# Kernel optimization log

Measured on AMD Instinct MI355X. Metric: run time of the kernel, lower is better.

## Reference

```python
import jax, jax.numpy as jnp
import numpy as np

# dims (match init_kwargs)
T, B, N, D_OB = 256, 32, 64, 4
D_MODEL = N * D_OB            # 256
D_PE = 16
D_T = D_MODEL + D_PE          # 272 transformer width
H = 8
DH = D_T // H                 # 34
L = 2
DFF = 1024
C = 2
MAX_LEN = T
F_IN = T * D_OB               # 1024, ObservationPropagation channels


def setup_inputs() -> dict:
    key = jax.random.key(0)
    ks = jax.random.split(key, 24)
    g = lambda k, shp: 0.02 * jax.random.normal(k, shp, dtype=jnp.float32)
    return {
        "x": jax.random.normal(ks[0], (T, B, N), dtype=jnp.float32),
        "times": jnp.sort(jax.random.uniform(ks[1], (T, B), dtype=jnp.float32) * MAX_LEN, axis=0),
        "lengths": jax.random.randint(ks[2], (B,), MAX_LEN // 2, MAX_LEN + 1),
        "R_u": g(ks[3], (1, N * D_OB)),
        "Wv1": g(ks[4], (F_IN, F_IN)), "bv1": g(ks[5], (F_IN,)),
        "Wv2": g(ks[6], (F_IN, F_IN)), "bv2": g(ks[7], (F_IN,)),
        "qkv_w": g(ks[8], (L, D_T, 3 * D_T)), "qkv_b": g(ks[9], (L, 3 * D_T)),
        "out_w": g(ks[10], (L, D_T, D_T)), "out_b": g(ks[11], (L, D_T)),
        "ln1_w": jnp.ones((L, D_T), jnp.float32), "ln1_b": jnp.zeros((L, D_T), jnp.float32),
        "ln2_w": jnp.ones((L, D_T), jnp.float32), "ln2_b": jnp.zeros((L, D_T), jnp.float32),
        "ffn_w1": g(ks[12], (L, D_T, DFF)), "ffn_b1": g(ks[13], (L, DFF)),
        "ffn_w2": g(ks[14], (L, DFF, D_T)), "ffn_b2": g(ks[15], (L, D_T)),
        "mlp_w1": g(ks[16], (D_T, D_T)), "mlp_b1": g(ks[17], (D_T,)),
        "mlp_w2": g(ks[18], (D_T, C)), "mlp_b2": g(ks[19], (C,)),
    }


def _pos_encode(times):
    # PositionalEncodingTF: timescales = max_len ** linspace(0,1,d_pe//2)
    scales = MAX_LEN ** np.linspace(0.0, 1.0, D_PE // 2)
    st = times[..., None] / jnp.asarray(scales, times.dtype)  # [T,B,8]
    return jnp.concatenate([jnp.sin(st), jnp.cos(st)], axis=-1)  # [T,B,16]


def _segment_softmax(w, seg, num_segments):
    m = jax.ops.segment_max(w, seg, num_segments=num_segments)
    e = jnp.exp(w - m[seg])
    s = jax.ops.segment_sum(e, seg, num_segments=num_segments)
    return e / s[seg]


def _ob_propagate(xn, src, tgt, edge_w, Wv, bv):
    """Batched ObservationPropagation (use_beta=False, decompose=False).
    xn: [B,N,F]; messages = relu(lin_value(x_src)) * softmax(edge_w per target);
    scatter-add at targets. Returns (out, pre-softmax alpha == edge_w)."""
    gamma = _segment_softmax(edge_w, tgt, N)              # [E]
    value = jax.nn.relu(xn @ Wv + bv)                     # [B,N,F] (linear commutes with gather)
    msg = value[:, src, :] * gamma[None, :, None]         # [B,E,F] -- dominant memory traffic
    out = jnp.zeros_like(xn).at[:, tgt, :].add(msg)       # segment-sum at target nodes
    return out, edge_w


def _ln(x, w, b):
    mu = jnp.mean(x, axis=-1, keepdims=True)
    var = jnp.mean((x - mu) ** 2, axis=-1, keepdims=True)
    return (x - mu) / jnp.sqrt(var + 1e-5) * w + b


def _encoder_layer(xt, key_pad, qkv_w, qkv_b, out_w, out_b, ln1_w, ln1_b, ln2_w, ln2_b, w1, b1, w2, b2):
    # xt: [T,B,D_T]; key_pad: [B,T] True = padded. Post-norm torch TransformerEncoderLayer, relu, no dropout.
    Tt, Bb, _ = xt.shape
    q, k, v = jnp.split(xt @ qkv_w + qkv_b, 3, axis=-1)
    to_h = lambda t: t.reshape(Tt, Bb, H, DH).transpose(1, 2, 0, 3)  # [B,H,T,dh]
    scores = jnp.einsum("bhqd,bhkd->bhqk", to_h(q), to_h(k)) / jnp.sqrt(jnp.asarray(DH, xt.dtype))
    scores = jnp.where(key_pad[:, None, None, :], -jnp.inf, scores)
    attn = jax.nn.softmax(scores, axis=-1)
    o = jnp.einsum("bhqk,bhkd->bhqd", attn, to_h(v)).transpose(2, 0, 1, 3).reshape(Tt, Bb, D_T)
    xt = _ln(xt + o @ out_w + out_b, ln1_w, ln1_b)
    ff = jax.nn.relu(xt @ w1 + b1) @ w2 + b2
    return _ln(xt + ff, ln2_w, ln2_b)


def _forward(x, times, lengths, R_u, Wv1, bv1, Wv2, bv2, qkv_w, qkv_b, out_w, out_b,
             ln1_w, ln1_b, ln2_w, ln2_b, ffn_w1, ffn_b1, ffn_w2, ffn_b2,
             mlp_w1, mlp_b1, mlp_w2, mlp_b2):
    Bb = x.shape[1]
    # observation embedding: repeat each sensor d_ob times, scale by R_u, relu
    h = jax.nn.relu(jnp.repeat(x, D_OB, axis=-1) * R_u)          # [T,B,N*d_ob]
    pe = _pos_encode(times)                                      # [T,B,16]
    key_pad = jnp.arange(T)[None, :] >= lengths[:, None]         # [B,T]
    # reshape to per-sensor node features: [B, N, T*d_ob]
    xn = h.reshape(T, Bb, N, D_OB).transpose(1, 2, 0, 3).reshape(Bb, N, F_IN)
    # dense all-pairs graph (global_structure = ones); torch.nonzero order is row-major
    src = jnp.repeat(jnp.arange(N), N)   # edge_index[0]
    tgt = jnp.tile(jnp.arange(N), N)     # edge_index[1] (aggregation index)
    ew = jnp.ones((N * N,), x.dtype)
    xn, ew2 = _ob_propagate(xn, src, tgt, ew, Wv1, bv1)
    xn, _ = _ob_propagate(xn, src, tgt, ew2, Wv2, bv2)
    out = xn.reshape(Bb, N, T, D_OB).transpose(2, 0, 1, 3).reshape(T, Bb, N * D_OB)
    out = jnp.concatenate([out, pe], axis=2)                     # [T,B,272]
    for l in range(L):
        out = _encoder_layer(out, key_pad, qkv_w[l], qkv_b[l], out_w[l], out_b[l],
                             ln1_w[l], ln1_b[l], ln2_w[l], ln2_b[l],
                             ffn_w1[l], ffn_b1[l], ffn_w2[l], ffn_b2[l])
    keep = (~key_pad).T[:, :, None].astype(out.dtype)            # [T,B,1]
    agg = jnp.sum(out * keep, axis=0) / (lengths[:, None].astype(out.dtype) + 1.0)
    hid = jax.nn.relu(agg @ mlp_w1 + mlp_b1)
    logits = hid @ mlp_w2 + mlp_b2
    return jax.nn.softmax(logits, axis=1)                        # [B,C]


def reference(x, times, lengths, R_u, Wv1, bv1, Wv2, bv2, qkv_w, qkv_b, out_w, out_b,
              ln1_w, ln1_b, ln2_w, ln2_b, ffn_w1, ffn_b1, ffn_w2, ffn_b2,
              mlp_w1, mlp_b1, mlp_w2, mlp_b2):
    return _forward(x, times, lengths, R_u, Wv1, bv1, Wv2, bv2, qkv_w, qkv_b, out_w, out_b,
                    ln1_w, ln1_b, ln2_w, ln2_b, ffn_w1, ffn_b1, ffn_w2, ffn_b2,
                    mlp_w1, mlp_b1, mlp_w2, mlp_b2)
```

## Files before the change

### kernel.cpp

```cpp
#include <hip/hip_runtime.h>
#include <math.h>

#define T_DIM 256
#define B_DIM 32
#define N_DIM 64
#define F_INF 1024
#define D_T 272
#define D_TP 288
#define H_DIM 8
#define DH_DIM 34
#define DFF_DIM 1024

typedef unsigned int uint;
typedef short bf16x8 __attribute__((ext_vector_type(8)));
typedef float f32x4 __attribute__((ext_vector_type(4)));

__device__ __forceinline__ ushort f2bf(float f) {
    uint u = __float_as_uint(f);
    uint r = (u + 0x7fffu + ((u >> 16) & 1u)) >> 16;
    return (ushort)r;
}
__device__ __forceinline__ float bf2f(ushort u) {
    return __uint_as_float(((uint)u) << 16);
}

struct WT {
    int tstart[11];
    const float* src[10];
    ushort* dst[10];
    int K[10];
    int N[10];
    int Kp[10];
    int ntn[10];
};
__global__ __launch_bounds__(256) void wconv_tiled(WT s) {
    int tile = blockIdx.x;
    int seg = 0;
    while (seg < 9 && tile >= s.tstart[seg + 1]) ++seg;
    int ti = tile - s.tstart[seg];
    int ntn = s.ntn[seg];
    int tk = ti / ntn, tn = ti - tk * ntn;
    int N = s.N[seg], Kp = s.Kp[seg];
    __shared__ float t[16][17];
    int ty = threadIdx.x >> 4, tx = threadIdx.x & 15;
    t[ty][tx] = s.src[seg][(size_t)(tk * 16 + ty) * N + tn * 16 + tx];
    __syncthreads();
    s.dst[seg][(size_t)(tn * 16 + ty) * Kp + tk * 16 + tx] = f2bf(t[tx][ty]);
}

struct PadPtrs {
    uint* wt[6];
    int nrows[6];
};
__global__ void init_kernel(const float* __restrict__ x, const float* __restrict__ Ru,
                            ushort* __restrict__ xn, uint* __restrict__ qkvb,
                            uint* __restrict__ x1, uint* __restrict__ attno, PadPtrs p) {
    const int TB = T_DIM * B_DIM;
    const int NXN = B_DIM * N_DIM * F_INF;
    int idx = blockIdx.x * blockDim.x + threadIdx.x;
    if (idx < NXN) {
        int f = idx & 1023;
        int bn = idx >> 10;
        int n = bn & 63;
        int b = bn >> 6;
        int t = f >> 2;
        int d = f & 3;
        float v = x[(t * B_DIM + b) * N_DIM + n] * Ru[(n << 2) + d];
        xn[idx] = f2bf(fmaxf(v, 0.0f));
        return;
    }
    idx -= NXN;
    if (idx < TB * 8) {
        int row = idx >> 3, q = idx & 7;
        x1[(size_t)row * 144 + 136 + q] = 0;
        attno[(size_t)row * 144 + 136 + q] = 0;
        return;
    }
    idx -= TB * 8;
    if (idx < TB * 72) {
        int row = idx / 72;
        int r = idx - row * 72;
        int g = r / 3, q = r - g * 3;
        qkvb[(size_t)row * 480 + g * 20 + 17 + q] = 0;
        return;
    }
    idx -= TB * 72;
#pragma unroll
    for (int sgi = 0; sgi < 6; ++sgi) {
        int cnt = p.nrows[sgi] * 8;
        if (idx < cnt) {
            int row = idx >> 3, q = idx & 7;
            p.wt[sgi][(size_t)row * 144 + 136 + q] = 0;
            return;
        }
        idx -= cnt;
    }
}

template <int ACT, int OUT_MODE>
__global__ __launch_bounds__(256) void gemm_mfma(const ushort* __restrict__ A,
                                                 const ushort* __restrict__ Bt,
                                                 const float* __restrict__ bias,
                                                 void* __restrict__ Cout,
                                                 int M, int N, int K, int Kstride) {
    __shared__ ushort As[3][64 * 32];
    __shared__ ushort Bs[3][128 * 32];
    const int tid = threadIdx.x;
    const int m0 = (OUT_MODE == 3) ? 0 : blockIdx.y * 64;
    const int n0 = blockIdx.x * 128;
    if (OUT_MODE == 3) {
        A += (size_t)blockIdx.y * K;
        Bt += (size_t)blockIdx.y * K;
    }
    const int w = tid >> 6, lane = tid & 63;
    const int wr = w >> 1, wc = w & 1;
    const int lr = lane & 15, lk = lane >> 4;

    const int ns = K >> 5;

    const int ra = w * 16 + (lane >> 2);
    const int ca = (((lane & 3) ^ ((ra >> 1) & 3)) << 3);
    int gma = m0 + ra; if (gma > M - 1) gma = M - 1;
    const ushort* gA = &A[(size_t)gma * Kstride + ca];
    const int rb0 = w * 32 + (lane >> 2);
    const int cb0 = (((lane & 3) ^ ((rb0 >> 1) & 3)) << 3);
    const int rb1 = rb0 + 16;
    const int cb1 = (((lane & 3) ^ ((rb1 >> 1) & 3)) << 3);
    int gnb0 = n0 + rb0; if (gnb0 > N - 1) gnb0 = N - 1;
    int gnb1 = n0 + rb1; if (gnb1 > N - 1) gnb1 = N - 1;
    const ushort* gB0 = &Bt[(size_t)gnb0 * Kstride + cb0];
    const ushort* gB1 = &Bt[(size_t)gnb1 * Kstride + cb1];

    f32x4 acc[2][4];
#pragma unroll
    for (int i = 0; i < 2; ++i)
#pragma unroll
        for (int j = 0; j < 4; ++j) acc[i][j] = (f32x4){0.f, 0.f, 0.f, 0.f};

    auto stage = [&](int buf, int s) {
        const int k0 = s << 5;
        __builtin_amdgcn_global_load_lds(
            (const __attribute__((address_space(1))) void*)(gA + k0),
            (__attribute__((address_space(3))) void*)(&As[buf][w * 512]), 16, 0, 0);
        __builtin_amdgcn_global_load_lds(
            (const __attribute__((address_space(1))) void*)(gB0 + k0),
            (__attribute__((address_space(3))) void*)(&Bs[buf][w * 1024]), 16, 0, 0);
        __builtin_amdgcn_global_load_lds(
            (const __attribute__((address_space(1))) void*)(gB1 + k0),
            (__attribute__((address_space(3))) void*)(&Bs[buf][w * 1024 + 512]), 16, 0, 0);
    };

    stage(0, 0);
    stage(1, 1);
    asm volatile("s_waitcnt vmcnt(3)" ::: "memory");
    __builtin_amdgcn_sched_barrier(0);
    __builtin_amdgcn_s_barrier();
    __builtin_amdgcn_sched_barrier(0);

    int cur = 0;
    for (int s = 0; s < ns; ++s) {
        int stg = cur + 2; if (stg >= 3) stg -= 3;
        if (s + 2 < ns) stage(stg, s + 2);

        bf16x8 af[2], bf[4];
#pragma unroll
        for (int mt = 0; mt < 2; ++mt) {
            int row = wr * 32 + mt * 16 + lr;
            int ch = lk ^ ((row >> 1) & 3);
            af[mt] = *reinterpret_cast<const bf16x8*>(&As[cur][row * 32 + ch * 8]);
        }
#pragma unroll
        for (int nt = 0; nt < 4; ++nt) {
            int row = wc * 64 + nt * 16 + lr;
            int ch = lk ^ ((row >> 1) & 3);
            bf[nt] = *reinterpret_cast<const bf16x8*>(&Bs[cur][row * 32 + ch * 8]);
        }
        __builtin_amdgcn_s_setprio(1);
#pragma unroll
        for (int mt = 0; mt < 2; ++mt)
#pragma unroll
            for (int nt = 0; nt < 4; ++nt)
                acc[mt][nt] = __builtin_amdgcn_mfma_f32_16x16x32_bf16(
                    af[mt], bf[nt], acc[mt][nt], 0, 0, 0);
        __builtin_amdgcn_s_setprio(0);

        if (s + 1 < ns) {
            if (s + 2 < ns)
                asm volatile("s_waitcnt vmcnt(3)" ::: "memory");
            else
                asm volatile("s_waitcnt vmcnt(0)" ::: "memory");
            __builtin_amdgcn_sched_barrier(0);
            __builtin_amdgcn_s_barrier();
            __builtin_amdgcn_sched_barrier(0);
        }
        cur = (cur == 2) ? 0 : cur + 1;
    }

    if (OUT_MODE == 4) {
        __shared__ float red[2][128];
        float part[4];
#pragma unroll
        for (int nt = 0; nt < 4; ++nt) {
            int col = n0 + wc * 64 + nt * 16 + lr;
            float bv = bias[col];
            float s = 0.f;
#pragma unroll
            for (int mt = 0; mt < 2; ++mt)
#pragma unroll
                for (int r = 0; r < 4; ++r) s += fmaxf(acc[mt][nt][r] + bv, 0.f);
            s += __shfl_xor(s, 16);
            s += __shfl_xor(s, 32);
            part[nt] = s;
        }
        if (lk == 0) {
#pragma unroll
            for (int nt = 0; nt < 4; ++nt) red[wr][wc * 64 + nt * 16 + lr] = part[nt];
        }
        __syncthreads();
        if (tid < 128) {
            float tot = red[0][tid] + red[1][tid];
            ((ushort*)Cout)[(size_t)blockIdx.y * 1024 + n0 + tid] =
                f2bf(tot * (1.0f / 64.0f));
        }
        return;
    }

#pragma unroll
    for (int nt = 0; nt < 4; ++nt) {
        int col = n0 + wc * 64 + nt * 16 + lr;
        if (col >= N) continue;
        float bv = (OUT_MODE == 3) ? 0.f : bias[col];
        int g = 0, dcol = 0;
        if (OUT_MODE == 2) { g = col / 34; dcol = col - g * 34; }
#pragma unroll
        for (int mt = 0; mt < 2; ++mt) {
#pragma unroll
            for (int r = 0; r < 4; ++r) {
                int row = m0 + wr * 32 + mt * 16 + lk * 4 + r;
                if (row >= M) continue;
                float v = acc[mt][nt][r] + bv;
                if (ACT == 1) v = fmaxf(v, 0.0f);
                if (OUT_MODE == 0)
                    ((float*)Cout)[(size_t)row * N + col] = v;
                else if (OUT_MODE == 1)
                    ((ushort*)Cout)[(size_t)row * N + col] = f2bf(v);
                else if (OUT_MODE == 2)
                    ((ushort*)Cout)[(size_t)row * 960 + g * 40 + dcol] = f2bf(v);
                else
                    ((float*)Cout)[(size_t)(blockIdx.y * M + row) * N + col] = v;
            }
        }
    }
}

__global__ __launch_bounds__(256) void gemm_ln(const ushort* __restrict__ A,
                                               const ushort* __restrict__ Bt,
                                               const float* __restrict__ bias,
                                               const ushort* __restrict__ resid,
                                               const float* __restrict__ lnw,
                                               const float* __restrict__ lnb,
                                               ushort* __restrict__ Out,
                                               int K, int Kstride) {
    __shared__ ushort lds[32256];
    const int tid = threadIdx.x;
    const int m0 = blockIdx.x * 64;
    const int w = tid >> 6, lane = tid & 63;
    const int lr = lane & 15, lk = lane >> 4;
    const int ns = K >> 5;

    const int ra = w * 16 + (lane >> 2);
    const int ca = (((lane & 3) ^ ((ra >> 1) & 3)) << 3);
    const ushort* gA = &A[(size_t)(m0 + ra) * Kstride + ca];

    f32x4 acc[17];
#pragma unroll
    for (int t = 0; t < 17; ++t) acc[t] = (f32x4){0.f, 0.f, 0.f, 0.f};

    auto stage = [&](int buf, int s) {
        const int k0 = s << 5;
        __builtin_amdgcn_global_load_lds(
            (const __attribute__((address_space(1))) void*)(gA + k0),
            (__attribute__((address_space(3))) void*)(&lds[buf * 2048 + w * 512]),
            16, 0, 0);
        for (int c = w; c < 17; c += 4) {
            int row16 = c * 16 + (lane >> 2);
            int p8 = (((lane & 3) ^ ((row16 >> 1) & 3)) << 3);
            const ushort* src = &Bt[(size_t)row16 * Kstride + k0 + p8];
            __builtin_amdgcn_global_load_lds(
                (const __attribute__((address_space(1))) void*)src,
                (__attribute__((address_space(3))) void*)(&lds[6144 + buf * 8704 + c * 512]),
                16, 0, 0);
        }
    };

    stage(0, 0);
    stage(1, 1);
    if (w == 0)
        asm volatile("s_waitcnt vmcnt(6)" ::: "memory");
    else
        asm volatile("s_waitcnt vmcnt(5)" ::: "memory");
    __builtin_amdgcn_sched_barrier(0);
    __builtin_amdgcn_s_barrier();
    __builtin_amdgcn_sched_barrier(0);

    int cur = 0;
    for (int s = 0; s < ns; ++s) {
        int stg = cur + 2; if (stg >= 3) stg -= 3;
        if (s + 2 < ns) stage(stg, s + 2);

        bf16x8 af;
        {
            int row = w * 16 + lr;
            int ch = lk ^ ((row >> 1) & 3);
            af = *reinterpret_cast<const bf16x8*>(&lds[cur * 2048 + row * 32 + ch * 8]);
        }
        __builtin_amdgcn_s_setprio(1);
#pragma unroll
        for (int t = 0; t < 17; ++t) {
            int row = t * 16 + lr;
            int ch = lk ^ ((row >> 1) & 3);
            bf16x8 bf = *reinterpret_cast<const bf16x8*>(
                &lds[6144 + cur * 8704 + row * 32 + ch * 8]);
            acc[t] = __builtin_amdgcn_mfma_f32_16x16x32_bf16(af, bf, acc[t], 0, 0, 0);
        }
        __builtin_amdgcn_s_setprio(0);

        if (s + 1 < ns) {
            if (s + 2 < ns) {
                if (w == 0)
                    asm volatile("s_waitcnt vmcnt(6)" ::: "memory");
                else
                    asm volatile("s_waitcnt vmcnt(5)" ::: "memory");
            } else {
                asm volatile("s_waitcnt vmcnt(0)" ::: "memory");
            }
            __builtin_amdgcn_sched_barrier(0);
            __builtin_amdgcn_s_barrier();
            __builtin_amdgcn_sched_barrier(0);
        }
        cur = (cur == 2) ? 0 : cur + 1;
    }

    __syncthreads();
    for (int i = tid; i < 64 * 34; i += 256) {
        int row = i / 34, c8 = i - row * 34;
        *reinterpret_cast<uint4*>(&lds[row * 272 + c8 * 8]) =
            *reinterpret_cast<const uint4*>(&resid[(size_t)(m0 + row) * D_TP + c8 * 8]);
    }
    __syncthreads();

    float sum[4] = {0.f, 0.f, 0.f, 0.f}, sq[4] = {0.f, 0.f, 0.f, 0.f};
#pragma unroll
    for (int t = 0; t < 17; ++t) {
        int col = t * 16 + lr;
        float bv = bias[col];
#pragma unroll
        for (int r = 0; r < 4; ++r) {
            int row = w * 16 + lk * 4 + r;
            float v = acc[t][r] + bv + bf2f(lds[row * 272 + col]);
            acc[t][r] = v;
            sum[r] += v;
            sq[r] += v * v;
        }
    }
#pragma unroll
    for (int mask = 1; mask <= 8; mask <<= 1)
#pragma unroll
        for (int r = 0; r < 4; ++r) {
            sum[r] += __shfl_xor(sum[r], mask);
            sq[r] += __shfl_xor(sq[r], mask);
        }
    float mu[4], inv[4];
#pragma unroll
    for (int r = 0; r < 4; ++r) {
        mu[r] = sum[r] * (1.0f / D_T);
        float var = sq[r] * (1.0f / D_T) - mu[r] * mu[r];
        inv[r] = 1.0f / sqrtf(var + 1e-5f);
    }
#pragma unroll
    for (int t = 0; t < 17; ++t) {
        int col = t * 16 + lr;
        float wv = lnw[col], bb = lnb[col];
#pragma unroll
        for (int r = 0; r < 4; ++r) {
            int row = m0 + w * 16 + lk * 4 + r;
            Out[(size_t)row * D_TP + col] = f2bf((acc[t][r] - mu[r]) * inv[r] * wv + bb);
        }
    }
}

__global__ __launch_bounds__(256) void reduce_p2_kernel(const float* __restrict__ part,
                                                        const float* __restrict__ bv2,
                                                        float* __restrict__ out2) {
    int idx = blockIdx.x * 256 + threadIdx.x;
    if (idx >= B_DIM * F_INF) return;
    int g = idx & 1023;
    float s = bv2[g];
#pragma unroll
    for (int ks = 0; ks < 4; ++ks) s += part[(size_t)ks * B_DIM * F_INF + idx];
    out2[idx] = fmaxf(s, 0.f);
}

__global__ void seq_kernel(const float* __restrict__ out2, const float* __restrict__ times,
                           ushort* __restrict__ seq) {
    int idx = blockIdx.x * blockDim.x + threadIdx.x;
    if (idx >= T_DIM * B_DIM * D_TP) return;
    int c = idx % D_TP;
    int tb = idx / D_TP;
    float v;
    if (c < 256) {
        v = out2[(tb % B_DIM) * 1024 + ((tb / B_DIM) << 2) + (c & 3)];
    } else if (c < 272) {
        int s = c - 256;
        int sc = (s < 8) ? s : s - 8;
        float arg = times[tb] * exp2f(-8.0f * (float)sc * (1.0f / 7.0f));
        v = (s < 8) ? sinf(arg) : cosf(arg);
    } else {
        v = 0.f;
    }
    seq[idx] = f2bf(v);
}

__global__ __launch_bounds__(256) void attn_mfma(const ushort* __restrict__ qkv,
                                                 const int* __restrict__ lengths,
                                                 ushort* __restrict__ attno) {
    const int b = blockIdx.x >> 3;
    const int h = blockIdx.x & 7;
    const int tid = threadIdx.x;
    const int w = tid >> 6, lane = tid & 63;
    const int lr = lane & 15, lk = lane >> 4;
    __shared__ ushort Ks[2][64 * 40];
    __shared__ ushort Vt[2][48 * 72];
    __shared__ ushort Ps[4][64 * 72];
    const int len = lengths[b];
    const float scale = 0.1714985851f;
    const bf16x8 zv = {0, 0, 0, 0, 0, 0, 0, 0};

    for (int i = tid; i < 2 * 8 * 72; i += 256) {
        int bb = i / 576;
        Vt[bb][40 * 72 + (i - bb * 576)] = 0;
    }

    const int srow0 = tid / 5, sch0 = tid - srow0 * 5;
    const int srow1 = (tid + 256) / 5, sch1 = (tid + 256) - srow1 * 5;
    const int sjp0 = (srow0 & 15) * 4 + (srow0 >> 4);
    const int sjp1 = (srow1 & 15) * 4 + (srow1 >> 4);
    const bool has1 = (tid < 64);
    bf16x8 kreg0, kreg1, vreg0, vreg1;

    auto LOADS = [&](int c) {
        const ushort* b0 = &qkv[(size_t)((c * 64 + srow0) * 32 + b) * 960 + h * 40];
        kreg0 = *reinterpret_cast<const bf16x8*>(b0 + 320 + sch0 * 8);
        vreg0 = *reinterpret_cast<const bf16x8*>(b0 + 640 + sch0 * 8);
        if (has1) {
            const ushort* b1 = &qkv[(size_t)((c * 64 + srow1) * 32 + b) * 960 + h * 40];
            kreg1 = *reinterpret_cast<const bf16x8*>(b1 + 320 + sch1 * 8);
            vreg1 = *reinterpret_cast<const bf16x8*>(b1 + 640 + sch1 * 8);
        }
    };
    auto WRITES = [&](int buf) {
        *reinterpret_cast<bf16x8*>(&Ks[buf][srow0 * 40 + sch0 * 8]) = kreg0;
#pragma unroll
        for (int e = 0; e < 8; ++e) Vt[buf][(sch0 * 8 + e) * 72 + sjp0] = (ushort)vreg0[e];
        if (has1) {
            *reinterpret_cast<bf16x8*>(&Ks[buf][srow1 * 40 + sch1 * 8]) = kreg1;
#pragma unroll
            for (int e = 0; e < 8; ++e) Vt[buf][(sch1 * 8 + e) * 72 + sjp1] = (ushort)vreg1[e];
        }
    };

    bf16x8 qf0[4], qf1[4];
#pragma unroll
    for (int it = 0; it < 4; ++it) {
        int t = w * 64 + it * 16 + lr;
        const ushort* qrow = &qkv[(size_t)(t * 32 + b) * 960 + h * 40];
        qf0[it] = *reinterpret_cast<const bf16x8*>(qrow + lk * 8);
        qf1[it] = (lk == 0) ? *reinterpret_cast<const bf16x8*>(qrow + 32) : zv;
    }

    f32x4 oacc[4][3];
#pragma unroll
    for (int it = 0; it < 4; ++it)
#pragma unroll
        for (int dt = 0; dt < 3; ++dt) oacc[it][dt] = (f32x4){0.f, 0.f, 0.f, 0.f};
    float m[4][4], l[4][4];
#pragma unroll
    for (int it = 0; it < 4; ++it)
#pragma unroll
        for (int r = 0; r < 4; ++r) { m[it][r] = -1e30f; l[it][r] = 0.f; }

    const int nchunks = (len + 63) >> 6;
    LOADS(0);
    WRITES(0);
    __syncthreads();

    int cur = 0;
    for (int c = 0; c < nchunks; ++c) {
        const bool pre = (c + 1 < nchunks);
        if (pre) LOADS(c + 1);

        bf16x8 kf0[4], kf1[4];
#pragma unroll
        for (int jt = 0; jt < 4; ++jt) {
            int j = jt * 16 + lr;
            kf0[jt] = *reinterpret_cast<const bf16x8*>(&Ks[cur][j * 40 + lk * 8]);
            kf1[jt] = (lk == 0) ? *reinterpret_cast<const bf16x8*>(&Ks[cur][j * 40 + 32]) : zv;
        }

        const bool tail = (c * 64 + 64 > len);
#pragma unroll
        for (int it = 0; it < 4; ++it) {
            f32x4 sacc[4];
#pragma unroll
            for (int jt = 0; jt < 4; ++jt) sacc[jt] = (f32x4){0.f, 0.f, 0.f, 0.f};
            __builtin_amdgcn_s_setprio(1);
#pragma unroll
            for (int jt = 0; jt < 4; ++jt) {
                sacc[jt] = __builtin_amdgcn_mfma_f32_16x16x32_bf16(qf0[it], kf0[jt],
                                                                   sacc[jt], 0, 0, 0);
                sacc[jt] = __builtin_amdgcn_mfma_f32_16x16x32_bf16(qf1[it], kf1[jt],
                                                                   sacc[jt], 0, 0, 0);
            }
            __builtin_amdgcn_s_setprio(0);
            float cm[4] = {-1e30f, -1e30f, -1e30f, -1e30f};
#pragma unroll
            for (int jt = 0; jt < 4; ++jt) {
                bool dead = tail && (c * 64 + jt * 16 + lr >= len);
#pragma unroll
                for (int r = 0; r < 4; ++r) {
                    float sv = dead ? -1e30f : sacc[jt][r];
                    sacc[jt][r] = sv;
                    cm[r] = fmaxf(cm[r], sv);
                }
            }
#pragma unroll
            for (int mask = 1; mask <= 8; mask <<= 1)
#pragma unroll
                for (int r = 0; r < 4; ++r) cm[r] = fmaxf(cm[r], __shfl_xor(cm[r], mask));
#pragma unroll
            for (int r = 0; r < 4; ++r) {
                float mn = fmaxf(m[it][r], cm[r]);
                float corr = __expf((m[it][r] - mn) * scale);
                m[it][r] = mn;
                l[it][r] *= corr;
#pragma unroll
                for (int dt = 0; dt < 3; ++dt) oacc[it][dt][r] *= corr;
            }
            float ls[4] = {0.f, 0.f, 0.f, 0.f};
#pragma unroll
            for (int jt = 0; jt < 4; ++jt)
#pragma unroll
                for (int r = 0; r < 4; ++r) {
                    float e = __expf((sacc[jt][r] - m[it][r]) * scale);
                    sacc[jt][r] = e;
                    ls[r] += e;
                }
#pragma unroll
            for (int mask = 1; mask <= 8; mask <<= 1)
#pragma unroll
                for (int r = 0; r < 4; ++r) ls[r] += __shfl_xor(ls[r], mask);
#pragma unroll
            for (int r = 0; r < 4; ++r) l[it][r] += ls[r];
#pragma unroll
            for (int r = 0; r < 4; ++r) {
                int i = it * 16 + lk * 4 + r;
                uint u0 = (uint)f2bf(sacc[0][r]) | ((uint)f2bf(sacc[1][r]) << 16);
                uint u1 = (uint)f2bf(sacc[2][r]) | ((uint)f2bf(sacc[3][r]) << 16);
                uint2 pk = make_uint2(u0, u1);
                *reinterpret_cast<uint2*>(&Ps[w][i * 72 + lr * 4]) = pk;
            }
        }

        bf16x8 vf[3][2], pf[4][2];
#pragma unroll
        for (int dt = 0; dt < 3; ++dt)
#pragma unroll
            for (int ks = 0; ks < 2; ++ks)
                vf[dt][ks] = *reinterpret_cast<const bf16x8*>(
                    &Vt[cur][(dt * 16 + lr) * 72 + ks * 32 + lk * 8]);
#pragma unroll
        for (int it = 0; it < 4; ++it)
#pragma unroll
            for (int ks = 0; ks < 2; ++ks)
                pf[it][ks] = *reinterpret_cast<const bf16x8*>(
                    &Ps[w][(it * 16 + lr) * 72 + ks * 32 + lk * 8]);
        __builtin_amdgcn_s_setprio(1);
#pragma unroll
        for (int it = 0; it < 4; ++it)
#pragma unroll
            for (int dt = 0; dt < 3; ++dt)
#pragma unroll
                for (int ks = 0; ks < 2; ++ks)
                    oacc[it][dt] = __builtin_amdgcn_mfma_f32_16x16x32_bf16(
                        pf[it][ks], vf[dt][ks], oacc[it][dt], 0, 0, 0);
        __builtin_amdgcn_s_setprio(0);

        if (pre) WRITES(cur ^ 1);
        __syncthreads();
        cur ^= 1;
    }

#pragma unroll
    for (int it = 0; it < 4; ++it)
#pragma unroll
        for (int r = 0; r < 4; ++r) {
            float inv = 1.0f / l[it][r];
            int t = w * 64 + it * 16 + lk * 4 + r;
            ushort* orow = &attno[(size_t)(t * 32 + b) * D_TP + h * 34];
#pragma unroll
            for (int dt = 0; dt < 3; ++dt) {
                int d = dt * 16 + lr;
                if (d < 34) orow[d] = f2bf(oacc[it][dt][r] * inv);
            }
        }
}

__global__ __launch_bounds__(256) void pool_partial(const ushort* __restrict__ seq,
                                                    const int* __restrict__ lengths,
                                                    float* __restrict__ partial) {
    const int chunk = blockIdx.x;
    const int b = blockIdx.y;
    const int tid = threadIdx.x;
    if (tid >= 136) return;
    const int len = lengths[b];
    float s0 = 0.f, s1 = 0.f;
    int t0 = chunk * 32;
    int tmax = len - t0;
    if (tmax > 32) tmax = 32;
#pragma unroll 4
    for (int r = 0; r < tmax; ++r) {
        uint u = *reinterpret_cast<const uint*>(
            &seq[(size_t)((t0 + r) * B_DIM + b) * D_TP + tid * 2]);
        s0 += __uint_as_float(u << 16);
        s1 += __uint_as_float(u & 0xffff0000u);
    }
    float* p = &partial[(size_t)(chunk * B_DIM + b) * D_T + tid * 2];
    p[0] = s0;
    p[1] = s1;
}

__global__ __launch_bounds__(256) void head_kernel(const float* __restrict__ partial,
                                                   const int* __restrict__ lengths,
                                                   const float* __restrict__ w1,
                                                   const float* __restrict__ b1,
                                                   const float* __restrict__ w2,
                                                   const float* __restrict__ b2,
                                                   float* __restrict__ out) {
    const int b = blockIdx.x;
    const int tid = threadIdx.x;
    const int len = lengths[b];
    __shared__ float agg_s[D_T];
    __shared__ float hid[D_T];
    float inv = 1.0f / (float)(len + 1);
    for (int c = tid; c < D_T; c += 256) {
        float s = 0.f;
#pragma unroll
        for (int ch = 0; ch < 8; ++ch)
            s += partial[(size_t)(ch * B_DIM + b) * D_T + c];
        agg_s[c] = s * inv;
    }
    __syncthreads();
    for (int j = tid; j < D_T; j += 256) {
        float acc = b1[j];
        for (int k = 0; k < D_T; ++k) acc += agg_s[k] * w1[k * D_T + j];
        hid[j] = fmaxf(acc, 0.f);
    }
    __syncthreads();
    if (tid < 64) {
        float l0 = 0.f, l1 = 0.f;
        for (int k = tid; k < D_T; k += 64) {
            float hv = hid[k];
            l0 += hv * w2[k * 2 + 0];
            l1 += hv * w2[k * 2 + 1];
        }
#pragma unroll
        for (int off = 32; off; off >>= 1) {
            l0 += __shfl_down(l0, off);
            l1 += __shfl_down(l1, off);
        }
        if (tid == 0) {
            l0 += b2[0];
            l1 += b2[1];
            float mx = fmaxf(l0, l1);
            float e0 = expf(l0 - mx), e1 = expf(l1 - mx);
            float nrm = 1.0f / (e0 + e1);
            out[b * 2 + 0] = e0 * nrm;
            out[b * 2 + 1] = e1 * nrm;
        }
    }
}

extern "C" void kernel_launch(void* const* d_in, const int* in_sizes, int n_in,
                              void* d_out, int out_size, void* d_ws, size_t ws_size,
                              hipStream_t stream) {
    const float* x      = (const float*)d_in[0];
    const float* times  = (const float*)d_in[1];
    const int*   lens   = (const int*)d_in[2];
    const float* R_u    = (const float*)d_in[3];
    const float* Wv1    = (const float*)d_in[4];
    const float* bv1    = (const float*)d_in[5];
    const float* Wv2    = (const float*)d_in[6];
    const float* bv2    = (const float*)d_in[7];
    const float* qkv_w  = (const float*)d_in[8];
    const float* qkv_b  = (const float*)d_in[9];
    const float* out_w  = (const float*)d_in[10];
    const float* out_b  = (const float*)d_in[11];
    const float* ln1_w  = (const float*)d_in[12];
    const float* ln1_b  = (const float*)d_in[13];
    const float* ln2_w  = (const float*)d_in[14];
    const float* ln2_b  = (const float*)d_in[15];
    const float* ffn_w1 = (const float*)d_in[16];
    const float* ffn_b1 = (const float*)d_in[17];
    const float* ffn_w2 = (const float*)d_in[18];
    const float* ffn_b2 = (const float*)d_in[19];
    const float* mlp_w1 = (const float*)d_in[20];
    const float* mlp_b1 = (const float*)d_in[21];
    const float* mlp_w2 = (const float*)d_in[22];
    const float* mlp_b2 = (const float*)d_in[23];
    float* outp = (float*)d_out;

    char* base = (char*)d_ws;
    size_t used = 0;
    auto alloc = [&](size_t bytes) -> char* {
        char* p = base + used;
        used += (bytes + 255) & ~(size_t)255;
        return p;
    };
    const int TB = T_DIM * B_DIM;

    ushort* xn    = (ushort*)alloc((size_t)2048 * 1024 * 2);
    ushort* s1    = (ushort*)alloc((size_t)32 * 1024 * 2);
    float*  p2p   = (float*) alloc((size_t)4 * 32 * 1024 * 4);
    float*  out2  = (float*) alloc((size_t)32 * 1024 * 4);
    ushort* seq   = (ushort*)alloc((size_t)TB * D_TP * 2);
    ushort* qkvb  = (ushort*)alloc((size_t)TB * 960 * 2);
    ushort* attno = (ushort*)alloc((size_t)TB * D_TP * 2);
    ushort* x1    = (ushort*)alloc((size_t)TB * D_TP * 2);
    ushort* h1    = (ushort*)alloc((size_t)TB * DFF_DIM * 2);
    float*  ppart = (float*) alloc((size_t)8 * B_DIM * D_T * 4);
    ushort* wv1t  = (ushort*)alloc((size_t)1024 * 1024 * 2);
    ushort* wv2t  = (ushort*)alloc((size_t)1024 * 1024 * 2);
    ushort* qkvwt[2]; ushort* outwt[2]; ushort* f1wt[2]; ushort* f2wt[2];
    for (int l = 0; l < 2; ++l) {
        qkvwt[l] = (ushort*)alloc((size_t)816 * D_TP * 2);
        outwt[l] = (ushort*)alloc((size_t)272 * D_TP * 2);
        f1wt[l]  = (ushort*)alloc((size_t)1024 * D_TP * 2);
        f2wt[l]  = (ushort*)alloc((size_t)272 * 1024 * 2);
    }
    if (used > ws_size) return;

    {
        WT segs;
        const float* srcs[10] = {Wv1, Wv2,
                                 qkv_w, out_w, ffn_w1, ffn_w2,
                                 qkv_w + (size_t)272 * 816, out_w + (size_t)272 * 272,
                                 ffn_w1 + (size_t)272 * 1024, ffn_w2 + (size_t)1024 * 272};
        ushort* dsts[10] = {wv1t, wv2t, qkvwt[0], outwt[0], f1wt[0], f2wt[0],
                            qkvwt[1], outwt[1], f1wt[1], f2wt[1]};
        int Ksz[10] = {1024, 1024, 272, 272, 272, 1024, 272, 272, 272, 1024};
        int Nsz[10] = {1024, 1024, 816, 272, 1024, 272, 816, 272, 1024, 272};
        int Kpd[10] = {1024, 1024, D_TP, D_TP, D_TP, 1024, D_TP, D_TP, D_TP, 1024};
        int acc = 0;
        for (int i = 0; i < 10; ++i) {
            segs.tstart[i] = acc;
            segs.src[i] = srcs[i];
            segs.dst[i] = dsts[i];
            segs.K[i] = Ksz[i];
            segs.N[i] = Nsz[i];
            segs.Kp[i] = Kpd[i];
            segs.ntn[i] = Nsz[i] / 16;
            acc += (Ksz[i] / 16) * (Nsz[i] / 16);
        }
        segs.tstart[10] = acc;
        wconv_tiled<<<acc, 256, 0, stream>>>(segs);
    }

    {
        PadPtrs pp;
        pp.wt[0] = (uint*)qkvwt[0]; pp.nrows[0] = 816;
        pp.wt[1] = (uint*)qkvwt[1]; pp.nrows[1] = 816;
        pp.wt[2] = (uint*)outwt[0]; pp.nrows[2] = 272;
        pp.wt[3] = (uint*)outwt[1]; pp.nrows[3] = 272;
        pp.wt[4] = (uint*)f1wt[0];  pp.nrows[4] = 1024;
        pp.wt[5] = (uint*)f1wt[1];  pp.nrows[5] = 1024;
        int n = B_DIM * N_DIM * F_INF + TB * 8 + TB * 72 +
                (816 + 816 + 272 + 272 + 1024 + 1024) * 8;
        init_kernel<<<(n + 255) / 256, 256, 0, stream>>>(x, R_u, xn, (uint*)qkvb,
                                                         (uint*)x1, (uint*)attno, pp);
    }

    gemm_mfma<1, 4><<<dim3(8, 32), 256, 0, stream>>>(xn, wv1t, bv1, s1,
                                                     2048, 1024, 1024, 1024);
    gemm_mfma<0, 3><<<dim3(8, 4), 256, 0, stream>>>(s1, wv2t, nullptr, p2p,
                                                    32, 1024, 256, 1024);
    reduce_p2_kernel<<<128, 256, 0, stream>>>(p2p, bv2, out2);

    {
        int n = TB * D_TP;
        seq_kernel<<<(n + 255) / 256, 256, 0, stream>>>(out2, times, seq);
    }

    for (int l = 0; l < 2; ++l) {
        const float* qb  = qkv_b + (size_t)l * 816;
        const float* ob  = out_b + (size_t)l * D_T;
        const float* l1w = ln1_w + (size_t)l * D_T;
        const float* l1b = ln1_b + (size_t)l * D_T;
        const float* l2w = ln2_w + (size_t)l * D_T;
        const float* l2b = ln2_b + (size_t)l * D_T;
        const float* f1b = ffn_b1 + (size_t)l * DFF_DIM;
        const float* f2b = ffn_b2 + (size_t)l * D_T;

        gemm_mfma<0, 2><<<dim3(7, 128), 256, 0, stream>>>(seq, qkvwt[l], qb, qkvb,
                                                          TB, 816, D_TP, D_TP);
        attn_mfma<<<B_DIM * H_DIM, 256, 0, stream>>>(qkvb, lens, attno);
        gemm_ln<<<128, 256, 0, stream>>>(attno, outwt[l], ob, seq, l1w, l1b, x1,
                                         D_TP, D_TP);
        gemm_mfma<1, 1><<<dim3(8, 128), 256, 0, stream>>>(x1, f1wt[l], f1b, h1,
                                                          TB, DFF_DIM, D_TP, D_TP);
        gemm_ln<<<128, 256, 0, stream>>>(h1, f2wt[l], f2b, x1, l2w, l2b, seq,
                                         1024, 1024);
    }

    pool_partial<<<dim3(8, B_DIM), 256, 0, stream>>>(seq, lens, ppart);
    head_kernel<<<B_DIM, 256, 0, stream>>>(ppart, lens, mlp_w1, mlp_b1,
                                           mlp_w2, mlp_b2, outp);
}
```

Before: 288.1 us.

## Fuse out-proj+LN1 with FFN1 GEMM, merge init kernels, fold reduce into seq

```diff
diff --git a/kernel.cpp b/kernel.cpp
--- a/kernel.cpp
+++ b/kernel.cpp
@@ -28,44 +28,47 @@
     int tstart[11];
     const float* src[10];
     ushort* dst[10];
-    int K[10];
     int N[10];
     int Kp[10];
     int ntn[10];
 };
-__global__ __launch_bounds__(256) void wconv_tiled(WT s) {
-    int tile = blockIdx.x;
-    int seg = 0;
-    while (seg < 9 && tile >= s.tstart[seg + 1]) ++seg;
-    int ti = tile - s.tstart[seg];
-    int ntn = s.ntn[seg];
-    int tk = ti / ntn, tn = ti - tk * ntn;
-    int N = s.N[seg], Kp = s.Kp[seg];
-    __shared__ float t[16][17];
-    int ty = threadIdx.x >> 4, tx = threadIdx.x & 15;
-    t[ty][tx] = s.src[seg][(size_t)(tk * 16 + ty) * N + tn * 16 + tx];
-    __syncthreads();
-    s.dst[seg][(size_t)(tn * 16 + ty) * Kp + tk * 16 + tx] = f2bf(t[tx][ty]);
-}
-
 struct PadPtrs {
     uint* wt[6];
     int nrows[6];
 };
-__global__ void init_kernel(const float* __restrict__ x, const float* __restrict__ Ru,
-                            ushort* __restrict__ xn, uint* __restrict__ qkvb,
-                            uint* __restrict__ x1, uint* __restrict__ attno, PadPtrs p) {
+__global__ __launch_bounds__(256) void wconv_init(WT s, int ntiles,
+                                                  const float* __restrict__ x,
+                                                  const float* __restrict__ Ru,
+                                                  ushort* __restrict__ xn,
+                                                  uint* __restrict__ qkvb,
+                                                  uint* __restrict__ x1,
+                                                  uint* __restrict__ attno, PadPtrs p) {
+    __shared__ float t[16][17];
+    if ((int)blockIdx.x < ntiles) {
+        int tile = blockIdx.x;
+        int seg = 0;
+        while (seg < 9 && tile >= s.tstart[seg + 1]) ++seg;
+        int ti = tile - s.tstart[seg];
+        int ntn = s.ntn[seg];
+        int tk = ti / ntn, tn = ti - tk * ntn;
+        int N = s.N[seg], Kp = s.Kp[seg];
+        int ty = threadIdx.x >> 4, tx = threadIdx.x & 15;
+        t[ty][tx] = s.src[seg][(size_t)(tk * 16 + ty) * N + tn * 16 + tx];
+        __syncthreads();
+        s.dst[seg][(size_t)(tn * 16 + ty) * Kp + tk * 16 + tx] = f2bf(t[tx][ty]);
+        return;
+    }
     const int TB = T_DIM * B_DIM;
     const int NXN = B_DIM * N_DIM * F_INF;
-    int idx = blockIdx.x * blockDim.x + threadIdx.x;
+    int idx = (blockIdx.x - ntiles) * 256 + threadIdx.x;
     if (idx < NXN) {
         int f = idx & 1023;
         int bn = idx >> 10;
         int n = bn & 63;
         int b = bn >> 6;
-        int t = f >> 2;
+        int tt = f >> 2;
         int d = f & 3;
-        float v = x[(t * B_DIM + b) * N_DIM + n] * Ru[(n << 2) + d];
+        float v = x[(tt * B_DIM + b) * N_DIM + n] * Ru[(n << 2) + d];
         xn[idx] = f2bf(fmaxf(v, 0.0f));
         return;
     }
@@ -240,14 +243,253 @@
                 if (row >= M) continue;
                 float v = acc[mt][nt][r] + bv;
                 if (ACT == 1) v = fmaxf(v, 0.0f);
-                if (OUT_MODE == 0)
-                    ((float*)Cout)[(size_t)row * N + col] = v;
-                else if (OUT_MODE == 1)
+                if (OUT_MODE == 1)
                     ((ushort*)Cout)[(size_t)row * N + col] = f2bf(v);
                 else if (OUT_MODE == 2)
                     ((ushort*)Cout)[(size_t)row * 960 + g * 40 + dcol] = f2bf(v);
                 else
                     ((float*)Cout)[(size_t)(blockIdx.y * M + row) * N + col] = v;
+            }
+        }
+    }
+}
+
+#define YSTR 296
+#define RING 19456
+__global__ __launch_bounds__(256) void gemm_ln_ffn(const ushort* __restrict__ A,
+                                                   const ushort* __restrict__ Bt,
+                                                   const float* __restrict__ bias,
+                                                   const ushort* __restrict__ resid,
+                                                   const float* __restrict__ lnw,
+                                                   const float* __restrict__ lnb,
+                                                   ushort* __restrict__ X1out,
+                                                   const ushort* __restrict__ B2t,
+                                                   const float* __restrict__ bias2,
+                                                   ushort* __restrict__ H1out) {
+    __shared__ ushort lds[32256];
+    const int tid = threadIdx.x;
+    const int m0 = blockIdx.x * 64;
+    const int w = tid >> 6, lane = tid & 63;
+    const int lr = lane & 15, lk = lane >> 4;
+    const int ns = 9;
+
+    {
+        const int ra = w * 16 + (lane >> 2);
+        const int ca = (((lane & 3) ^ ((ra >> 1) & 3)) << 3);
+        const ushort* gA = &A[(size_t)(m0 + ra) * D_TP + ca];
+
+        f32x4 acc[17];
+#pragma unroll
+        for (int t = 0; t < 17; ++t) acc[t] = (f32x4){0.f, 0.f, 0.f, 0.f};
+
+        auto stage = [&](int buf, int s) {
+            const int k0 = s << 5;
+            __builtin_amdgcn_global_load_lds(
+                (const __attribute__((address_space(1))) void*)(gA + k0),
+                (__attribute__((address_space(3))) void*)(&lds[buf * 2048 + w * 512]),
+                16, 0, 0);
+            for (int c = w; c < 17; c += 4) {
+                int row16 = c * 16 + (lane >> 2);
+                int p8 = (((lane & 3) ^ ((row16 >> 1) & 3)) << 3);
+                const ushort* src = &Bt[(size_t)row16 * D_TP + k0 + p8];
+                __builtin_amdgcn_global_load_lds(
+                    (const __attribute__((address_space(1))) void*)src,
+                    (__attribute__((address_space(3))) void*)(&lds[6144 + buf * 8704 + c * 512]),
+                    16, 0, 0);
+            }
+        };
+
+        stage(0, 0);
+        stage(1, 1);
+        if (w == 0)
+            asm volatile("s_waitcnt vmcnt(6)" ::: "memory");
+        else
+            asm volatile("s_waitcnt vmcnt(5)" ::: "memory");
+        __builtin_amdgcn_sched_barrier(0);
+        __builtin_amdgcn_s_barrier();
+        __builtin_amdgcn_sched_barrier(0);
+
+        int cur = 0;
+        for (int s = 0; s < ns; ++s) {
+            int stg = cur + 2; if (stg >= 3) stg -= 3;
+            if (s + 2 < ns) stage(stg, s + 2);
+
+            bf16x8 af;
+            {
+                int row = w * 16 + lr;
+                int ch = lk ^ ((row >> 1) & 3);
+                af = *reinterpret_cast<const bf16x8*>(&lds[cur * 2048 + row * 32 + ch * 8]);
+            }
+            __builtin_amdgcn_s_setprio(1);
+#pragma unroll
+            for (int t = 0; t < 17; ++t) {
+                int row = t * 16 + lr;
+                int ch = lk ^ ((row >> 1) & 3);
+                bf16x8 bf = *reinterpret_cast<const bf16x8*>(
+                    &lds[6144 + cur * 8704 + row * 32 + ch * 8]);
+                acc[t] = __builtin_amdgcn_mfma_f32_16x16x32_bf16(af, bf, acc[t], 0, 0, 0);
+            }
+            __builtin_amdgcn_s_setprio(0);
+
+            if (s + 1 < ns) {
+                if (s + 2 < ns) {
+                    if (w == 0)
+                        asm volatile("s_waitcnt vmcnt(6)" ::: "memory");
+                    else
+                        asm volatile("s_waitcnt vmcnt(5)" ::: "memory");
+                } else {
+                    asm volatile("s_waitcnt vmcnt(0)" ::: "memory");
+                }
+                __builtin_amdgcn_sched_barrier(0);
+                __builtin_amdgcn_s_barrier();
+                __builtin_amdgcn_sched_barrier(0);
+            }
+            cur = (cur == 2) ? 0 : cur + 1;
+        }
+
+        __syncthreads();
+        for (int i = tid; i < 64 * 34; i += 256) {
+            int row = i / 34, c8 = i - row * 34;
+            *reinterpret_cast<uint4*>(&lds[row * 272 + c8 * 8]) =
+                *reinterpret_cast<const uint4*>(&resid[(size_t)(m0 + row) * D_TP + c8 * 8]);
+        }
+        __syncthreads();
+
+        float sum[4] = {0.f, 0.f, 0.f, 0.f}, sq[4] = {0.f, 0.f, 0.f, 0.f};
+#pragma unroll
+        for (int t = 0; t < 17; ++t) {
+            int col = t * 16 + lr;
+            float bv = bias[col];
+#pragma unroll
+            for (int r = 0; r < 4; ++r) {
+                int row = w * 16 + lk * 4 + r;
+                float v = acc[t][r] + bv + bf2f(lds[row * 272 + col]);
+                acc[t][r] = v;
+                sum[r] += v;
+                sq[r] += v * v;
+            }
+        }
+#pragma unroll
+        for (int mask = 1; mask <= 8; mask <<= 1)
+#pragma unroll
+            for (int r = 0; r < 4; ++r) {
+                sum[r] += __shfl_xor(sum[r], mask);
+                sq[r] += __shfl_xor(sq[r], mask);
+            }
+        float mu[4], inv[4];
+#pragma unroll
+        for (int r = 0; r < 4; ++r) {
+            mu[r] = sum[r] * (1.0f / D_T);
+            float var = sq[r] * (1.0f / D_T) - mu[r] * mu[r];
+            inv[r] = 1.0f / sqrtf(var + 1e-5f);
+        }
+        __syncthreads();
+#pragma unroll
+        for (int t = 0; t < 17; ++t) {
+            int col = t * 16 + lr;
+            float wv = lnw[col], bb = lnb[col];
+#pragma unroll
+            for (int r = 0; r < 4; ++r) {
+                int row = w * 16 + lk * 4 + r;
+                ushort val = f2bf((acc[t][r] - mu[r]) * inv[r] * wv + bb);
+                X1out[(size_t)(m0 + row) * D_TP + col] = val;
+                lds[row * YSTR + col] = val;
+            }
+        }
+        for (int i = tid; i < 64 * 16; i += 256) {
+            int row = i >> 4, q = i & 15;
+            lds[row * YSTR + 272 + q] = 0;
+        }
+        __syncthreads();
+    }
+
+    {
+        const int wr = w >> 1, wc = w & 1;
+        const int rb0 = w * 32 + (lane >> 2);
+        const int cb0 = (((lane & 3) ^ ((rb0 >> 1) & 3)) << 3);
+        const int rb1 = rb0 + 16;
+        const int cb1 = (((lane & 3) ^ ((rb1 >> 1) & 3)) << 3);
+
+        for (int chunk = 0; chunk < 8; ++chunk) {
+            const ushort* gB0 = &B2t[(size_t)(chunk * 128 + rb0) * D_TP + cb0];
+            const ushort* gB1 = &B2t[(size_t)(chunk * 128 + rb1) * D_TP + cb1];
+            auto stageB = [&](int buf, int s) {
+                const int k0 = s << 5;
+                __builtin_amdgcn_global_load_lds(
+                    (const __attribute__((address_space(1))) void*)(gB0 + k0),
+                    (__attribute__((address_space(3))) void*)(&lds[RING + buf * 4096 + w * 1024]),
+                    16, 0, 0);
+                __builtin_amdgcn_global_load_lds(
+                    (const __attribute__((address_space(1))) void*)(gB1 + k0),
+                    (__attribute__((address_space(3))) void*)(&lds[RING + buf * 4096 + w * 1024 + 512]),
+                    16, 0, 0);
+            };
+
+            f32x4 accb[2][4];
+#pragma unroll
+            for (int i = 0; i < 2; ++i)
+#pragma unroll
+                for (int j = 0; j < 4; ++j) accb[i][j] = (f32x4){0.f, 0.f, 0.f, 0.f};
+
+            stageB(0, 0);
+            stageB(1, 1);
+            asm volatile("s_waitcnt vmcnt(2)" ::: "memory");
+            __builtin_amdgcn_sched_barrier(0);
+            __builtin_amdgcn_s_barrier();
+            __builtin_amdgcn_sched_barrier(0);
+
+            int cur = 0;
+            for (int s = 0; s < 9; ++s) {
+                int stg = cur + 2; if (stg >= 3) stg -= 3;
+                if (s + 2 < 9) stageB(stg, s + 2);
+
+                bf16x8 af2[2], bf2[4];
+#pragma unroll
+                for (int mt = 0; mt < 2; ++mt) {
+                    int row = wr * 32 + mt * 16 + lr;
+                    af2[mt] = *reinterpret_cast<const bf16x8*>(
+                        &lds[row * YSTR + (s << 5) + lk * 8]);
+                }
+#pragma unroll
+                for (int nt = 0; nt < 4; ++nt) {
+                    int rowb = wc * 64 + nt * 16 + lr;
+                    int ch = lk ^ ((rowb >> 1) & 3);
+                    bf2[nt] = *reinterpret_cast<const bf16x8*>(
+                        &lds[RING + cur * 4096 + rowb * 32 + ch * 8]);
+                }
+                __builtin_amdgcn_s_setprio(1);
+#pragma unroll
+                for (int mt = 0; mt < 2; ++mt)
+#pragma unroll
+                    for (int nt = 0; nt < 4; ++nt)
+                        accb[mt][nt] = __builtin_amdgcn_mfma_f32_16x16x32_bf16(
+                            af2[mt], bf2[nt], accb[mt][nt], 0, 0, 0);
+                __builtin_amdgcn_s_setprio(0);
+
+                if (s + 1 < 9) {
+                    if (s + 2 < 9)
+                        asm volatile("s_waitcnt vmcnt(2)" ::: "memory");
+                    else
+                        asm volatile("s_waitcnt vmcnt(0)" ::: "memory");
+                    __builtin_amdgcn_sched_barrier(0);
+                    __builtin_amdgcn_s_barrier();
+                    __builtin_amdgcn_sched_barrier(0);
+                }
+                cur = (cur == 2) ? 0 : cur + 1;
+            }
+
+#pragma unroll
+            for (int nt = 0; nt < 4; ++nt) {
+                int col = chunk * 128 + wc * 64 + nt * 16 + lr;
+                float bv = bias2[col];
+#pragma unroll
+                for (int mt = 0; mt < 2; ++mt)
+#pragma unroll
+                    for (int r = 0; r < 4; ++r) {
+                        int row = m0 + wr * 32 + mt * 16 + lk * 4 + r;
+                        H1out[(size_t)row * 1024 + col] =
+                            f2bf(fmaxf(accb[mt][nt][r] + bv, 0.f));
+                    }
             }
         }
     }
@@ -389,27 +631,21 @@
     }
 }
 
-__global__ __launch_bounds__(256) void reduce_p2_kernel(const float* __restrict__ part,
-                                                        const float* __restrict__ bv2,
-                                                        float* __restrict__ out2) {
-    int idx = blockIdx.x * 256 + threadIdx.x;
-    if (idx >= B_DIM * F_INF) return;
-    int g = idx & 1023;
-    float s = bv2[g];
-#pragma unroll
-    for (int ks = 0; ks < 4; ++ks) s += part[(size_t)ks * B_DIM * F_INF + idx];
-    out2[idx] = fmaxf(s, 0.f);
-}
-
-__global__ void seq_kernel(const float* __restrict__ out2, const float* __restrict__ times,
-                           ushort* __restrict__ seq) {
+__global__ void seq_kernel(const float* __restrict__ p2p, const float* __restrict__ bv2,
+                           const float* __restrict__ times, ushort* __restrict__ seq) {
     int idx = blockIdx.x * blockDim.x + threadIdx.x;
     if (idx >= T_DIM * B_DIM * D_TP) return;
     int c = idx % D_TP;
     int tb = idx / D_TP;
     float v;
     if (c < 256) {
-        v = out2[(tb % B_DIM) * 1024 + ((tb / B_DIM) << 2) + (c & 3)];
+        int b = tb % B_DIM;
+        int g = ((tb / B_DIM) << 2) + (c & 3);
+        float s = bv2[g];
+#pragma unroll
+        for (int ks = 0; ks < 4; ++ks)
+            s += p2p[(size_t)(ks * B_DIM + b) * F_INF + g];
+        v = fmaxf(s, 0.f);
     } else if (c < 272) {
         int s = c - 256;
         int sc = (s < 8) ? s : s - 8;
@@ -731,7 +967,6 @@
     ushort* xn    = (ushort*)alloc((size_t)2048 * 1024 * 2);
     ushort* s1    = (ushort*)alloc((size_t)32 * 1024 * 2);
     float*  p2p   = (float*) alloc((size_t)4 * 32 * 1024 * 4);
-    float*  out2  = (float*) alloc((size_t)32 * 1024 * 4);
     ushort* seq   = (ushort*)alloc((size_t)TB * D_TP * 2);
     ushort* qkvb  = (ushort*)alloc((size_t)TB * 960 * 2);
     ushort* attno = (ushort*)alloc((size_t)TB * D_TP * 2);
@@ -765,17 +1000,13 @@
             segs.tstart[i] = acc;
             segs.src[i] = srcs[i];
             segs.dst[i] = dsts[i];
-            segs.K[i] = Ksz[i];
             segs.N[i] = Nsz[i];
             segs.Kp[i] = Kpd[i];
             segs.ntn[i] = Nsz[i] / 16;
             acc += (Ksz[i] / 16) * (Nsz[i] / 16);
         }
         segs.tstart[10] = acc;
-        wconv_tiled<<<acc, 256, 0, stream>>>(segs);
-    }
-
-    {
+
         PadPtrs pp;
         pp.wt[0] = (uint*)qkvwt[0]; pp.nrows[0] = 816;
         pp.wt[1] = (uint*)qkvwt[1]; pp.nrows[1] = 816;
@@ -783,21 +1014,20 @@
         pp.wt[3] = (uint*)outwt[1]; pp.nrows[3] = 272;
         pp.wt[4] = (uint*)f1wt[0];  pp.nrows[4] = 1024;
         pp.wt[5] = (uint*)f1wt[1];  pp.nrows[5] = 1024;
-        int n = B_DIM * N_DIM * F_INF + TB * 8 + TB * 72 +
-                (816 + 816 + 272 + 272 + 1024 + 1024) * 8;
-        init_kernel<<<(n + 255) / 256, 256, 0, stream>>>(x, R_u, xn, (uint*)qkvb,
-                                                         (uint*)x1, (uint*)attno, pp);
+        int ninit = B_DIM * N_DIM * F_INF + TB * 8 + TB * 72 +
+                    (816 + 816 + 272 + 272 + 1024 + 1024) * 8;
+        int nblk = acc + (ninit + 255) / 256;
+        wconv_init<<<nblk, 256, 0, stream>>>(segs, acc, x, R_u, xn, (uint*)qkvb,
+                                             (uint*)x1, (uint*)attno, pp);
     }
 
     gemm_mfma<1, 4><<<dim3(8, 32), 256, 0, stream>>>(xn, wv1t, bv1, s1,
                                                      2048, 1024, 1024, 1024);
     gemm_mfma<0, 3><<<dim3(8, 4), 256, 0, stream>>>(s1, wv2t, nullptr, p2p,
                                                     32, 1024, 256, 1024);
-    reduce_p2_kernel<<<128, 256, 0, stream>>>(p2p, bv2, out2);
-
     {
         int n = TB * D_TP;
-        seq_kernel<<<(n + 255) / 256, 256, 0, stream>>>(out2, times, seq);
+        seq_kernel<<<(n + 255) / 256, 256, 0, stream>>>(p2p, bv2, times, seq);
     }
 
     for (int l = 0; l < 2; ++l) {
@@ -813,10 +1043,8 @@
         gemm_mfma<0, 2><<<dim3(7, 128), 256, 0, stream>>>(seq, qkvwt[l], qb, qkvb,
                                                           TB, 816, D_TP, D_TP);
         attn_mfma<<<B_DIM * H_DIM, 256, 0, stream>>>(qkvb, lens, attno);
-        gemm_ln<<<128, 256, 0, stream>>>(attno, outwt[l], ob, seq, l1w, l1b, x1,
-                                         D_TP, D_TP);
-        gemm_mfma<1, 1><<<dim3(8, 128), 256, 0, stream>>>(x1, f1wt[l], f1b, h1,
-                                                          TB, DFF_DIM, D_TP, D_TP);
+        gemm_ln_ffn<<<128, 256, 0, stream>>>(attno, outwt[l], ob, seq, l1w, l1b, x1,
+                                             f1wt[l], f1b, h1);
         gemm_ln<<<128, 256, 0, stream>>>(h1, f2wt[l], f2b, x1, l2w, l2b, seq,
                                          1024, 1024);
     }
```

After: 294.2 us. +2.1%, slower.
